# Kernel tuning notes

Measured on AMD Instinct MI355X. Metric: run time of the kernel, lower is better.

The kernel has to match this reference:

```python
import jax, jax.numpy as jnp
import numpy as np

N_NODES = 40000
N_EDGES = 640000
DIM_H = 512
N_HEADS = 8
D_HEAD = DIM_H // N_HEADS


def setup_inputs() -> dict:
    key = jax.random.key(0)
    ks = jax.random.split(key, 8)
    x = jax.random.normal(ks[0], (N_NODES, DIM_H), dtype=jnp.float32)
    edge_index = jax.random.randint(ks[1], (2, N_EDGES), 0, N_NODES, dtype=jnp.int32)
    virt_h = jax.random.normal(ks[2], (1, DIM_H), dtype=jnp.float32)
    virt_edge_index = jnp.zeros((2, 1), dtype=jnp.int32)
    s = 1.0 / np.sqrt(DIM_H)
    Wq = jax.random.normal(ks[3], (DIM_H, DIM_H), dtype=jnp.float32) * s
    Wk = jax.random.normal(ks[4], (DIM_H, DIM_H), dtype=jnp.float32) * s
    Wv = jax.random.normal(ks[5], (DIM_H, DIM_H), dtype=jnp.float32) * s
    bn_gamma = jnp.ones((DIM_H,), dtype=jnp.float32)
    bn_beta = jnp.zeros((DIM_H,), dtype=jnp.float32)
    return {"x": x, "edge_index": edge_index, "virt_h": virt_h,
            "virt_edge_index": virt_edge_index, "Wq": Wq, "Wk": Wk, "Wv": Wv,
            "bn_gamma": bn_gamma, "bn_beta": bn_beta}


def _exphormer_attn(x, edge_index, Wq, Wk, Wv):
    N, D = x.shape
    H, d = N_HEADS, D_HEAD
    Q = (x @ Wq).reshape(N, H, d)
    K = (x @ Wk).reshape(N, H, d)
    V = (x @ Wv).reshape(N, H, d)
    src, dst = edge_index[0], edge_index[1]
    scale = np.float32(1.0 / np.sqrt(d))
    # per-edge, per-head score: sum over head dim of elementwise q*k
    score = jnp.einsum('ehd,ehd->eh', K[src], Q[dst]) * scale  # [E, H]
    score = jnp.exp(jnp.clip(score, -5.0, 5.0))[..., None]     # [E, H, 1]
    msg = V[src] * score                                        # [E, H, d]
    wV = jax.ops.segment_sum(msg, dst, num_segments=N)          # [N, H, d]
    Z = jax.ops.segment_sum(score, dst, num_segments=N)         # [N, H, 1]
    return (wV / (Z + 1e-6)).reshape(N, D)


def reference(x, edge_index, virt_h, virt_edge_index, Wq, Wk, Wv, bn_gamma, bn_beta):
    # virt_h / virt_edge_index unused: use_virt_nodes=False
    h_attn = _exphormer_attn(x, edge_index, Wq, Wk, Wv)
    h = x + h_attn  # dropout p=0 -> identity; residual
    # BatchNorm1d (training-mode batch statistics, biased variance)
    mean = jnp.mean(h, axis=0)
    var = jnp.mean(jnp.square(h - mean), axis=0)
    return (h - mean) * jax.lax.rsqrt(var + 1e-5) * bn_gamma + bn_beta
```

## Files before the change

kernel.cpp:

```cpp
#include <hip/hip_runtime.h>
#include <hip/hip_bf16.h>

#define N_NODES 40000
#define M_PAD   40064
#define N_EDGES 640000
#define DIM_H 512
#define QKV_STRIDE 1536
#define ROW_BYTES 3072

typedef __attribute__((ext_vector_type(8))) short bf16x8_t;
typedef __attribute__((ext_vector_type(4))) float f32x4_t;
typedef __attribute__((ext_vector_type(8))) unsigned short u16x8_t;

static __device__ __forceinline__ unsigned short f2bf(float f) {
    __hip_bfloat16 h = __float2bfloat16(f);
    return *reinterpret_cast<unsigned short*>(&h);
}
static __device__ __forceinline__ float bf2f(unsigned short u) {
    return __uint_as_float(((unsigned)u) << 16);
}
static __device__ __forceinline__ void gll16(const void* g, void* l) {
    __builtin_amdgcn_global_load_lds(
        (const __attribute__((address_space(1))) unsigned int*)g,
        (__attribute__((address_space(3))) unsigned int*)l, 16, 0, 0);
}

__global__ __launch_bounds__(256)
void cast_x(const float* __restrict__ x, unsigned short* __restrict__ xb)
{
    const size_t i = ((size_t)blockIdx.x * 256 + threadIdx.x) * 8;
    const float4 v0 = *(const float4*)&x[i];
    const float4 v1 = *(const float4*)&x[i + 4];
    u16x8_t o;
    o[0] = f2bf(v0.x); o[1] = f2bf(v0.y); o[2] = f2bf(v0.z); o[3] = f2bf(v0.w);
    o[4] = f2bf(v1.x); o[5] = f2bf(v1.y); o[6] = f2bf(v1.z); o[7] = f2bf(v1.w);
    *(u16x8_t*)&xb[i] = o;
}

__global__ __launch_bounds__(256)
void cast_wt(const float* __restrict__ Wq,
             const float* __restrict__ Wk,
             const float* __restrict__ Wv,
             unsigned short* __restrict__ Wt)
{
    __shared__ float tile[32][33];
    const float* W = (blockIdx.z == 0) ? Wq : (blockIdx.z == 1) ? Wk : Wv;
    unsigned short* Wo = Wt + (size_t)blockIdx.z * 512 * 512;
    const int k0 = blockIdx.x * 32, n0 = blockIdx.y * 32;
    const int tx = threadIdx.x & 31, ty0 = threadIdx.x >> 5;
    #pragma unroll
    for (int p = 0; p < 4; ++p) {
        const int r = ty0 + p * 8;
        tile[r][tx] = W[(size_t)(k0 + r) * 512 + n0 + tx];
    }
    __syncthreads();
    #pragma unroll
    for (int p = 0; p < 4; ++p) {
        const int r = ty0 + p * 8;
        Wo[(size_t)(n0 + r) * 512 + k0 + tx] = f2bf(tile[tx][r]);
    }
}

__global__ __launch_bounds__(256)
void qkv_gemm_mfma(const unsigned short* __restrict__ xb,
                   const unsigned short* __restrict__ Wt,
                   unsigned short* __restrict__ qkv)
{
    __shared__ short Asub[128 * 32];
    __shared__ short Bsub[128 * 32];

    const int orig = blockIdx.x;
    const int q = 469, rmod = 4;
    const int xcd = orig & 7;
    const int sub = orig >> 3;
    const int wg = (xcd < rmod ? xcd * (q + 1) : rmod * (q + 1) + (xcd - rmod) * q) + sub;
    const int n0g = (wg % 12) * 128;
    const int m0  = (wg / 12) * 128;

    const int wsel = n0g >> 9;
    const int nc0  = n0g & 511;
    const int tid = threadIdx.x;
    const int l = tid & 63;
    const int w = tid >> 6;
    const int wr = w >> 1, wc = w & 1;
    const int lr = l & 15;
    const int lk = (l >> 4) * 8;

    const int idx0 = tid, idx1 = 256 + tid;
    const int ar0 = idx0 >> 2, ac0 = (((idx0 & 3) ^ ((idx0 >> 3) & 3))) * 8;
    const int ar1 = idx1 >> 2, ac1 = (((idx1 & 3) ^ ((idx1 >> 3) & 3))) * 8;

    const unsigned short* Abase = xb + (size_t)m0 * 512;
    const unsigned short* Bbase = Wt + (size_t)wsel * 262144 + (size_t)nc0 * 512;

    f32x4_t acc[4][4];
    #pragma unroll
    for (int i = 0; i < 4; ++i)
        #pragma unroll
        for (int j = 0; j < 4; ++j)
            acc[i][j] = {0.f, 0.f, 0.f, 0.f};

    for (int k0 = 0; k0 < 512; k0 += 32) {
        gll16(Abase + (size_t)ar0 * 512 + k0 + ac0, &Asub[idx0 * 8]);
        gll16(Abase + (size_t)ar1 * 512 + k0 + ac1, &Asub[idx1 * 8]);
        gll16(Bbase + (size_t)ar0 * 512 + k0 + ac0, &Bsub[idx0 * 8]);
        gll16(Bbase + (size_t)ar1 * 512 + k0 + ac1, &Bsub[idx1 * 8]);
        __syncthreads();
        bf16x8_t a[4], b[4];
        #pragma unroll
        for (int fm = 0; fm < 4; ++fm) {
            const int Ra = wr * 64 + fm * 16 + lr;
            const int pa = (((lk >> 3) ^ ((Ra >> 1) & 3))) << 3;
            a[fm] = *(const bf16x8_t*)&Asub[Ra * 32 + pa];
        }
        #pragma unroll
        for (int fn = 0; fn < 4; ++fn) {
            const int Rb = wc * 64 + fn * 16 + lr;
            const int pb = (((lk >> 3) ^ ((Rb >> 1) & 3))) << 3;
            b[fn] = *(const bf16x8_t*)&Bsub[Rb * 32 + pb];
        }
        #pragma unroll
        for (int fm = 0; fm < 4; ++fm)
            #pragma unroll
            for (int fn = 0; fn < 4; ++fn)
                acc[fm][fn] = __builtin_amdgcn_mfma_f32_16x16x32_bf16(
                                  a[fm], b[fn], acc[fm][fn], 0, 0, 0);
        __syncthreads();
    }

    #pragma unroll
    for (int fm = 0; fm < 4; ++fm)
        #pragma unroll
        for (int fn = 0; fn < 4; ++fn)
            #pragma unroll
            for (int j = 0; j < 4; ++j) {
                const int row = m0 + wr * 64 + fm * 16 + (l >> 4) * 4 + j;
                const int col = n0g + wc * 64 + fn * 16 + lr;
                qkv[(size_t)row * QKV_STRIDE + col] = f2bf(acc[fm][fn][j]);
            }
}

__global__ __launch_bounds__(256)
void csr_hist(const int* __restrict__ ei, int* __restrict__ counts)
{
    const int e = blockIdx.x * 256 + threadIdx.x;
    atomicAdd(&counts[ei[N_EDGES + e]], 1);
}

__global__ __launch_bounds__(1024)
void csr_scan(const int* __restrict__ counts, int* __restrict__ row_ptr)
{
    __shared__ int part[1024];
    const int t = threadIdx.x;
    const int base = t * 40;
    int s = 0;
    for (int i = 0; i < 40; ++i) {
        const int idx = base + i;
        if (idx < N_NODES) s += counts[idx];
    }
    part[t] = s;
    __syncthreads();
    for (int off = 1; off < 1024; off <<= 1) {
        int v = (t >= off) ? part[t - off] : 0;
        __syncthreads();
        part[t] += v;
        __syncthreads();
    }
    int run = (t == 0) ? 0 : part[t - 1];
    for (int i = 0; i < 40; ++i) {
        const int idx = base + i;
        if (idx < N_NODES) { row_ptr[idx] = run; run += counts[idx]; }
    }
    if (t == 0) row_ptr[N_NODES] = part[1023];
}

__global__ __launch_bounds__(256)
void csr_scatter(const int* __restrict__ ei, const int* __restrict__ row_ptr,
                 int* __restrict__ cursor, unsigned short* __restrict__ col)
{
    const int e = blockIdx.x * 256 + threadIdx.x;
    const int dst = ei[N_EDGES + e];
    const int pos = atomicAdd(&cursor[dst], 1);
    col[row_ptr[dst] + pos] = (unsigned short)ei[e];
}

__global__ __launch_bounds__(256)
void quant_kv(unsigned short* __restrict__ qkv,
              float* __restrict__ kscale, float* __restrict__ vscale)
{
    const int node = blockIdx.x * 4 + (threadIdx.x >> 6);
    const int lane = threadIdx.x & 63;
    unsigned short* row = qkv + (size_t)node * QKV_STRIDE;

    const u16x8_t kk = *(const u16x8_t*)(row + 512 + lane * 8);
    const u16x8_t vv = *(const u16x8_t*)(row + 1024 + lane * 8);
    float kf[8], vf[8];
    float kamax = 0.f, vamax = 0.f;
    #pragma unroll
    for (int j = 0; j < 8; ++j) {
        kf[j] = bf2f(kk[j]); kamax = fmaxf(kamax, fabsf(kf[j]));
        vf[j] = bf2f(vv[j]); vamax = fmaxf(vamax, fabsf(vf[j]));
    }
    #pragma unroll
    for (int off = 1; off < 64; off <<= 1) {
        kamax = fmaxf(kamax, __shfl_xor(kamax, off, 64));
        vamax = fmaxf(vamax, __shfl_xor(vamax, off, 64));
    }
    const float kinv = (kamax > 0.f) ? 127.0f / kamax : 0.f;
    const float vinv = (vamax > 0.f) ? 127.0f / vamax : 0.f;

    unsigned int klo = 0, khi = 0, vlo = 0, vhi = 0;
    #pragma unroll
    for (int j = 0; j < 4; ++j) {
        const int kq = (int)rintf(kf[j] * kinv);
        const int vq = (int)rintf(vf[j] * vinv);
        klo |= ((unsigned)(unsigned char)(signed char)kq) << (8 * j);
        vlo |= ((unsigned)(unsigned char)(signed char)vq) << (8 * j);
    }
    #pragma unroll
    for (int j = 4; j < 8; ++j) {
        const int kq = (int)rintf(kf[j] * kinv);
        const int vq = (int)rintf(vf[j] * vinv);
        khi |= ((unsigned)(unsigned char)(signed char)kq) << (8 * (j - 4));
        vhi |= ((unsigned)(unsigned char)(signed char)vq) << (8 * (j - 4));
    }
    uint2 kp; kp.x = klo; kp.y = khi;
    uint2 vp; vp.x = vlo; vp.y = vhi;
    char* rowb = (char*)row;
    *(uint2*)(rowb + 1024 + lane * 8) = kp;
    *(uint2*)(rowb + 2048 + lane * 8) = vp;
    if (lane == 0) {
        kscale[node] = kamax * (1.0f / 127.0f);
        vscale[node] = vamax * (1.0f / 127.0f);
    }
}

__global__ __launch_bounds__(128)
void edge_fused(const unsigned short* __restrict__ qkv,
                const float* __restrict__ kscale,
                const float* __restrict__ vscale,
                const int* __restrict__ row_ptr,
                const unsigned short* __restrict__ col,
                const float* __restrict__ x,
                float* __restrict__ out)
{
    const int node = blockIdx.x * 2 + (threadIdx.x >> 6);
    const int lane = threadIdx.x & 63;
    const int d0b = lane * 8;

    const u16x8_t q8 = *(const u16x8_t*)(qkv + (size_t)node * QKV_STRIDE + lane * 8);
    float q[8];
    #pragma unroll
    for (int j = 0; j < 8; ++j) q[j] = bf2f(q8[j]);

    const char* qb = (const char*)qkv;
    float acc[8] = {0.f, 0.f, 0.f, 0.f, 0.f, 0.f, 0.f, 0.f};
    float zsum = 0.f;
    const int start = row_ptr[node];
    const int end   = row_ptr[node + 1];

    int e = start;
    for (; e + 4 <= end; e += 4) {
        const int s0 = col[e], s1 = col[e + 1], s2 = col[e + 2], s3 = col[e + 3];
        const uint2 k0 = *(const uint2*)(qb + (size_t)s0 * ROW_BYTES + 1024 + d0b);
        const uint2 k1 = *(const uint2*)(qb + (size_t)s1 * ROW_BYTES + 1024 + d0b);
        const uint2 k2 = *(const uint2*)(qb + (size_t)s2 * ROW_BYTES + 1024 + d0b);
        const uint2 k3 = *(const uint2*)(qb + (size_t)s3 * ROW_BYTES + 1024 + d0b);
        const uint2 v0 = *(const uint2*)(qb + (size_t)s0 * ROW_BYTES + 2048 + d0b);
        const uint2 v1 = *(const uint2*)(qb + (size_t)s1 * ROW_BYTES + 2048 + d0b);
        const uint2 v2 = *(const uint2*)(qb + (size_t)s2 * ROW_BYTES + 2048 + d0b);
        const uint2 v3 = *(const uint2*)(qb + (size_t)s3 * ROW_BYTES + 2048 + d0b);
        const signed char* ck0 = (const signed char*)&k0;
        const signed char* ck1 = (const signed char*)&k1;
        const signed char* ck2 = (const signed char*)&k2;
        const signed char* ck3 = (const signed char*)&k3;
        float p0 = 0.f, p1 = 0.f, p2 = 0.f, p3 = 0.f;
        #pragma unroll
        for (int j = 0; j < 8; ++j) {
            p0 = fmaf((float)ck0[j], q[j], p0);
            p1 = fmaf((float)ck1[j], q[j], p1);
            p2 = fmaf((float)ck2[j], q[j], p2);
            p3 = fmaf((float)ck3[j], q[j], p3);
        }
        p0 += __shfl_xor(p0, 1, 64); p0 += __shfl_xor(p0, 2, 64); p0 += __shfl_xor(p0, 4, 64);
        p1 += __shfl_xor(p1, 1, 64); p1 += __shfl_xor(p1, 2, 64); p1 += __shfl_xor(p1, 4, 64);
        p2 += __shfl_xor(p2, 1, 64); p2 += __shfl_xor(p2, 2, 64); p2 += __shfl_xor(p2, 4, 64);
        p3 += __shfl_xor(p3, 1, 64); p3 += __shfl_xor(p3, 2, 64); p3 += __shfl_xor(p3, 4, 64);
        const float sc0 = __expf(fminf(fmaxf(p0 * kscale[s0] * 0.125f, -5.f), 5.f));
        const float sc1 = __expf(fminf(fmaxf(p1 * kscale[s1] * 0.125f, -5.f), 5.f));
        const float sc2 = __expf(fminf(fmaxf(p2 * kscale[s2] * 0.125f, -5.f), 5.f));
        const float sc3 = __expf(fminf(fmaxf(p3 * kscale[s3] * 0.125f, -5.f), 5.f));
        zsum += (sc0 + sc1) + (sc2 + sc3);
        const float scv0 = sc0 * vscale[s0];
        const float scv1 = sc1 * vscale[s1];
        const float scv2 = sc2 * vscale[s2];
        const float scv3 = sc3 * vscale[s3];
        const signed char* cv0 = (const signed char*)&v0;
        const signed char* cv1 = (const signed char*)&v1;
        const signed char* cv2 = (const signed char*)&v2;
        const signed char* cv3 = (const signed char*)&v3;
        #pragma unroll
        for (int j = 0; j < 8; ++j) {
            float a = acc[j];
            a = fmaf(scv0, (float)cv0[j], a);
            a = fmaf(scv1, (float)cv1[j], a);
            a = fmaf(scv2, (float)cv2[j], a);
            a = fmaf(scv3, (float)cv3[j], a);
            acc[j] = a;
        }
    }
    for (; e < end; ++e) {
        const int s0 = col[e];
        const uint2 k0 = *(const uint2*)(qb + (size_t)s0 * ROW_BYTES + 1024 + d0b);
        const uint2 v0 = *(const uint2*)(qb + (size_t)s0 * ROW_BYTES + 2048 + d0b);
        const signed char* ck0 = (const signed char*)&k0;
        float p0 = 0.f;
        #pragma unroll
        for (int j = 0; j < 8; ++j) p0 = fmaf((float)ck0[j], q[j], p0);
        p0 += __shfl_xor(p0, 1, 64); p0 += __shfl_xor(p0, 2, 64); p0 += __shfl_xor(p0, 4, 64);
        const float sc0 = __expf(fminf(fmaxf(p0 * kscale[s0] * 0.125f, -5.f), 5.f));
        zsum += sc0;
        const float scv0 = sc0 * vscale[s0];
        const signed char* cv0 = (const signed char*)&v0;
        #pragma unroll
        for (int j = 0; j < 8; ++j) acc[j] = fmaf(scv0, (float)cv0[j], acc[j]);
    }

    const float invz = 1.0f / (zsum + 1e-6f);
    const float* xr = x + (size_t)node * 512 + lane * 8;
    float xv[8];
    #pragma unroll
    for (int j = 0; j < 8; ++j) xv[j] = __builtin_nontemporal_load(xr + j);
    float* orow = out + (size_t)node * 512 + lane * 8;
    #pragma unroll
    for (int j = 0; j < 8; ++j)
        __builtin_nontemporal_store(xv[j] + acc[j] * invz, orow + j);
}

__global__ __launch_bounds__(512)
void stats_pass(const float* __restrict__ hbuf, float* __restrict__ stats)
{
    const int c  = threadIdx.x;
    const int r0 = blockIdx.x * 80;
    float sum = 0.f, sq = 0.f;
    for (int i = 0; i < 80; ++i) {
        const float hv = hbuf[(size_t)(r0 + i) * 512 + c];
        sum += hv; sq += hv * hv;
    }
    atomicAdd(&stats[c], sum);
    atomicAdd(&stats[512 + c], sq);
}

__global__ __launch_bounds__(256)
void bn_norm(float* __restrict__ hbuf,
             const float* __restrict__ stats,
             const float* __restrict__ gamma,
             const float* __restrict__ beta)
{
    const size_t i4 = ((size_t)blockIdx.x * 256 + threadIdx.x) * 4;
    const int c = (int)(i4 & 511);
    const float invN = 1.0f / 40000.0f;
    float4 h = *(float4*)&hbuf[i4];
    float hv[4] = {h.x, h.y, h.z, h.w};
    float o[4];
    #pragma unroll
    for (int j = 0; j < 4; ++j) {
        const float mean = stats[c + j] * invN;
        const float var  = stats[512 + c + j] * invN - mean * mean;
        o[j] = (hv[j] - mean) * rsqrtf(var + 1e-5f) * gamma[c + j] + beta[c + j];
    }
    float4 out = {o[0], o[1], o[2], o[3]};
    *(float4*)&hbuf[i4] = out;
}

extern "C" void kernel_launch(void* const* d_in, const int* in_sizes, int n_in,
                              void* d_out, int out_size, void* d_ws, size_t ws_size,
                              hipStream_t stream)
{
    const float* x     = (const float*)d_in[0];
    const int*   ei    = (const int*)d_in[1];
    const float* Wq    = (const float*)d_in[4];
    const float* Wk    = (const float*)d_in[5];
    const float* Wv    = (const float*)d_in[6];
    const float* gamma = (const float*)d_in[7];
    const float* beta  = (const float*)d_in[8];
    float* out = (float*)d_out;

    char* ws = (char*)d_ws;
    unsigned short* qkv    = (unsigned short*)ws;
    unsigned short* xb     = (unsigned short*)(ws + 123076608);
    unsigned short* Wt     = (unsigned short*)(ws + 164102144);
    int*            counts = (int*)           (ws + 165675008);
    int*            cursor = (int*)           (ws + 165835008);
    int*            row_ptr= (int*)           (ws + 165995008);
    unsigned short* col    = (unsigned short*)(ws + 166155024);
    float*          stats  = (float*)         (ws + 167435056);
    float* kscale = (float*)(ws + 123076608 + 26000000);
    float* vscale = (float*)(ws + 123076608 + 26160000);

    hipMemsetAsync(counts, 0, 160000, stream);
    hipMemsetAsync(cursor, 0, 160000, stream);
    hipMemsetAsync(stats,  0, 4096,   stream);
    hipMemsetAsync(xb + (size_t)N_NODES * 512, 0, (size_t)(M_PAD - N_NODES) * 512 * 2, stream);

    cast_x<<<10000, 256, 0, stream>>>(x, xb);
    cast_wt<<<dim3(16, 16, 3), 256, 0, stream>>>(Wq, Wk, Wv, Wt);
    csr_hist<<<2500, 256, 0, stream>>>(ei, counts);
    csr_scan<<<1, 1024, 0, stream>>>(counts, row_ptr);
    csr_scatter<<<2500, 256, 0, stream>>>(ei, row_ptr, cursor, col);
    qkv_gemm_mfma<<<3756, 256, 0, stream>>>(xb, Wt, qkv);
    quant_kv<<<10000, 256, 0, stream>>>(qkv, kscale, vscale);
    edge_fused<<<20000, 128, 0, stream>>>(qkv, kscale, vscale, row_ptr, col, x, out);
    stats_pass<<<500, 512, 0, stream>>>(out, stats);
    bn_norm<<<20000, 256, 0, stream>>>(out, stats, gamma, beta);
}
```

Before: 442.9 us.

## Fuse K/V int8 quantization into GEMM epilogue with per-head scales in row

Removes the separate quant_kv kernel by quantizing K and V to int8 directly in the QKV GEMM epilogue, using per-head (64-wide) absmax scales reduced by lane shuffles. The scales are stored inside each node's row next to the int8 data, so edge_fused reads them from the same cache lines as K/V instead of from separate scale arrays. This saves a full read and write pass over the QKV buffer and some scattered scale loads. The scale granularity changes from per-node to per-head, which is finer and should slightly improve accuracy, but the epilogue now does byte-wide scattered stores.

```diff
diff --git a/kernel.cpp b/kernel.cpp
--- a/kernel.cpp
+++ b/kernel.cpp
@@ -128,16 +128,45 @@
         __syncthreads();
     }
 
-    #pragma unroll
-    for (int fm = 0; fm < 4; ++fm)
-        #pragma unroll
-        for (int fn = 0; fn < 4; ++fn)
+    if (wsel == 0) {
+        #pragma unroll
+        for (int fm = 0; fm < 4; ++fm)
+            #pragma unroll
+            for (int fn = 0; fn < 4; ++fn)
+                #pragma unroll
+                for (int j = 0; j < 4; ++j) {
+                    const int row = m0 + wr * 64 + fm * 16 + (l >> 4) * 4 + j;
+                    const int col = n0g + wc * 64 + fn * 16 + lr;
+                    qkv[(size_t)row * QKV_STRIDE + col] = f2bf(acc[fm][fn][j]);
+                }
+    } else {
+        const int hd     = (nc0 >> 6) + wc;
+        const int sbase  = (wsel == 1) ? 1024 : 2048;
+        const int scbase = (wsel == 1) ? 1536 : 1568;
+        #pragma unroll
+        for (int fm = 0; fm < 4; ++fm)
             #pragma unroll
             for (int j = 0; j < 4; ++j) {
                 const int row = m0 + wr * 64 + fm * 16 + (l >> 4) * 4 + j;
-                const int col = n0g + wc * 64 + fn * 16 + lr;
-                qkv[(size_t)row * QKV_STRIDE + col] = f2bf(acc[fm][fn][j]);
+                float m = 0.f;
+                #pragma unroll
+                for (int fn = 0; fn < 4; ++fn)
+                    m = fmaxf(m, fabsf(acc[fm][fn][j]));
+                m = fmaxf(m, __shfl_xor(m, 1, 64));
+                m = fmaxf(m, __shfl_xor(m, 2, 64));
+                m = fmaxf(m, __shfl_xor(m, 4, 64));
+                m = fmaxf(m, __shfl_xor(m, 8, 64));
+                const float inv = (m > 0.f) ? 127.0f / m : 0.f;
+                char* rowb = (char*)qkv + (size_t)row * ROW_BYTES;
+                #pragma unroll
+                for (int fn = 0; fn < 4; ++fn) {
+                    const int qv = (int)rintf(acc[fm][fn][j] * inv);
+                    rowb[sbase + hd * 64 + fn * 16 + lr] = (char)(signed char)qv;
+                }
+                if (lr == 0)
+                    *(float*)(rowb + scbase + hd * 4) = m * (1.0f / 127.0f);
             }
+    }
 }
 
 __global__ __launch_bounds__(256)
@@ -184,61 +213,8 @@
     col[row_ptr[dst] + pos] = (unsigned short)ei[e];
 }
 
-__global__ __launch_bounds__(256)
-void quant_kv(unsigned short* __restrict__ qkv,
-              float* __restrict__ kscale, float* __restrict__ vscale)
-{
-    const int node = blockIdx.x * 4 + (threadIdx.x >> 6);
-    const int lane = threadIdx.x & 63;
-    unsigned short* row = qkv + (size_t)node * QKV_STRIDE;
-
-    const u16x8_t kk = *(const u16x8_t*)(row + 512 + lane * 8);
-    const u16x8_t vv = *(const u16x8_t*)(row + 1024 + lane * 8);
-    float kf[8], vf[8];
-    float kamax = 0.f, vamax = 0.f;
-    #pragma unroll
-    for (int j = 0; j < 8; ++j) {
-        kf[j] = bf2f(kk[j]); kamax = fmaxf(kamax, fabsf(kf[j]));
-        vf[j] = bf2f(vv[j]); vamax = fmaxf(vamax, fabsf(vf[j]));
-    }
-    #pragma unroll
-    for (int off = 1; off < 64; off <<= 1) {
-        kamax = fmaxf(kamax, __shfl_xor(kamax, off, 64));
-        vamax = fmaxf(vamax, __shfl_xor(vamax, off, 64));
-    }
-    const float kinv = (kamax > 0.f) ? 127.0f / kamax : 0.f;
-    const float vinv = (vamax > 0.f) ? 127.0f / vamax : 0.f;
-
-    unsigned int klo = 0, khi = 0, vlo = 0, vhi = 0;
-    #pragma unroll
-    for (int j = 0; j < 4; ++j) {
-        const int kq = (int)rintf(kf[j] * kinv);
-        const int vq = (int)rintf(vf[j] * vinv);
-        klo |= ((unsigned)(unsigned char)(signed char)kq) << (8 * j);
-        vlo |= ((unsigned)(unsigned char)(signed char)vq) << (8 * j);
-    }
-    #pragma unroll
-    for (int j = 4; j < 8; ++j) {
-        const int kq = (int)rintf(kf[j] * kinv);
-        const int vq = (int)rintf(vf[j] * vinv);
-        khi |= ((unsigned)(unsigned char)(signed char)kq) << (8 * (j - 4));
-        vhi |= ((unsigned)(unsigned char)(signed char)vq) << (8 * (j - 4));
-    }
-    uint2 kp; kp.x = klo; kp.y = khi;
-    uint2 vp; vp.x = vlo; vp.y = vhi;
-    char* rowb = (char*)row;
-    *(uint2*)(rowb + 1024 + lane * 8) = kp;
-    *(uint2*)(rowb + 2048 + lane * 8) = vp;
-    if (lane == 0) {
-        kscale[node] = kamax * (1.0f / 127.0f);
-        vscale[node] = vamax * (1.0f / 127.0f);
-    }
-}
-
 __global__ __launch_bounds__(128)
 void edge_fused(const unsigned short* __restrict__ qkv,
-                const float* __restrict__ kscale,
-                const float* __restrict__ vscale,
                 const int* __restrict__ row_ptr,
                 const unsigned short* __restrict__ col,
                 const float* __restrict__ x,
@@ -246,6 +222,7 @@
 {
     const int node = blockIdx.x * 2 + (threadIdx.x >> 6);
     const int lane = threadIdx.x & 63;
+    const int g = lane >> 3;
     const int d0b = lane * 8;
 
     const u16x8_t q8 = *(const u16x8_t*)(qkv + (size_t)node * QKV_STRIDE + lane * 8);
@@ -262,14 +239,22 @@
     int e = start;
     for (; e + 4 <= end; e += 4) {
         const int s0 = col[e], s1 = col[e + 1], s2 = col[e + 2], s3 = col[e + 3];
-        const uint2 k0 = *(const uint2*)(qb + (size_t)s0 * ROW_BYTES + 1024 + d0b);
-        const uint2 k1 = *(const uint2*)(qb + (size_t)s1 * ROW_BYTES + 1024 + d0b);
-        const uint2 k2 = *(const uint2*)(qb + (size_t)s2 * ROW_BYTES + 1024 + d0b);
-        const uint2 k3 = *(const uint2*)(qb + (size_t)s3 * ROW_BYTES + 1024 + d0b);
-        const uint2 v0 = *(const uint2*)(qb + (size_t)s0 * ROW_BYTES + 2048 + d0b);
-        const uint2 v1 = *(const uint2*)(qb + (size_t)s1 * ROW_BYTES + 2048 + d0b);
-        const uint2 v2 = *(const uint2*)(qb + (size_t)s2 * ROW_BYTES + 2048 + d0b);
-        const uint2 v3 = *(const uint2*)(qb + (size_t)s3 * ROW_BYTES + 2048 + d0b);
+        const char* rb0 = qb + (size_t)s0 * ROW_BYTES;
+        const char* rb1 = qb + (size_t)s1 * ROW_BYTES;
+        const char* rb2 = qb + (size_t)s2 * ROW_BYTES;
+        const char* rb3 = qb + (size_t)s3 * ROW_BYTES;
+        const uint2 k0 = *(const uint2*)(rb0 + 1024 + d0b);
+        const uint2 k1 = *(const uint2*)(rb1 + 1024 + d0b);
+        const uint2 k2 = *(const uint2*)(rb2 + 1024 + d0b);
+        const uint2 k3 = *(const uint2*)(rb3 + 1024 + d0b);
+        const uint2 v0 = *(const uint2*)(rb0 + 2048 + d0b);
+        const uint2 v1 = *(const uint2*)(rb1 + 2048 + d0b);
+        const uint2 v2 = *(const uint2*)(rb2 + 2048 + d0b);
+        const uint2 v3 = *(const uint2*)(rb3 + 2048 + d0b);
+        const float ks0 = *(const float*)(rb0 + 1536 + g * 4);
+        const float ks1 = *(const float*)(rb1 + 1536 + g * 4);
+        const float ks2 = *(const float*)(rb2 + 1536 + g * 4);
+        const float ks3 = *(const float*)(rb3 + 1536 + g * 4);
         const signed char* ck0 = (const signed char*)&k0;
         const signed char* ck1 = (const signed char*)&k1;
         const signed char* ck2 = (const signed char*)&k2;
@@ -286,15 +271,15 @@
         p1 += __shfl_xor(p1, 1, 64); p1 += __shfl_xor(p1, 2, 64); p1 += __shfl_xor(p1, 4, 64);
         p2 += __shfl_xor(p2, 1, 64); p2 += __shfl_xor(p2, 2, 64); p2 += __shfl_xor(p2, 4, 64);
         p3 += __shfl_xor(p3, 1, 64); p3 += __shfl_xor(p3, 2, 64); p3 += __shfl_xor(p3, 4, 64);
-        const float sc0 = __expf(fminf(fmaxf(p0 * kscale[s0] * 0.125f, -5.f), 5.f));
-        const float sc1 = __expf(fminf(fmaxf(p1 * kscale[s1] * 0.125f, -5.f), 5.f));
-        const float sc2 = __expf(fminf(fmaxf(p2 * kscale[s2] * 0.125f, -5.f), 5.f));
-        const float sc3 = __expf(fminf(fmaxf(p3 * kscale[s3] * 0.125f, -5.f), 5.f));
+        const float sc0 = __expf(fminf(fmaxf(p0 * ks0 * 0.125f, -5.f), 5.f));
+        const float sc1 = __expf(fminf(fmaxf(p1 * ks1 * 0.125f, -5.f), 5.f));
+        const float sc2 = __expf(fminf(fmaxf(p2 * ks2 * 0.125f, -5.f), 5.f));
+        const float sc3 = __expf(fminf(fmaxf(p3 * ks3 * 0.125f, -5.f), 5.f));
         zsum += (sc0 + sc1) + (sc2 + sc3);
-        const float scv0 = sc0 * vscale[s0];
-        const float scv1 = sc1 * vscale[s1];
-        const float scv2 = sc2 * vscale[s2];
-        const float scv3 = sc3 * vscale[s3];
+        const float scv0 = sc0 * *(const float*)(rb0 + 1568 + g * 4);
+        const float scv1 = sc1 * *(const float*)(rb1 + 1568 + g * 4);
+        const float scv2 = sc2 * *(const float*)(rb2 + 1568 + g * 4);
+        const float scv3 = sc3 * *(const float*)(rb3 + 1568 + g * 4);
         const signed char* cv0 = (const signed char*)&v0;
         const signed char* cv1 = (const signed char*)&v1;
         const signed char* cv2 = (const signed char*)&v2;
@@ -311,16 +296,18 @@
     }
     for (; e < end; ++e) {
         const int s0 = col[e];
-        const uint2 k0 = *(const uint2*)(qb + (size_t)s0 * ROW_BYTES + 1024 + d0b);
-        const uint2 v0 = *(const uint2*)(qb + (size_t)s0 * ROW_BYTES + 2048 + d0b);
+        const char* rb0 = qb + (size_t)s0 * ROW_BYTES;
+        const uint2 k0 = *(const uint2*)(rb0 + 1024 + d0b);
+        const uint2 v0 = *(const uint2*)(rb0 + 2048 + d0b);
+        const float ks0 = *(const float*)(rb0 + 1536 + g * 4);
         const signed char* ck0 = (const signed char*)&k0;
         float p0 = 0.f;
         #pragma unroll
         for (int j = 0; j < 8; ++j) p0 = fmaf((float)ck0[j], q[j], p0);
         p0 += __shfl_xor(p0, 1, 64); p0 += __shfl_xor(p0, 2, 64); p0 += __shfl_xor(p0, 4, 64);
-        const float sc0 = __expf(fminf(fmaxf(p0 * kscale[s0] * 0.125f, -5.f), 5.f));
+        const float sc0 = __expf(fminf(fmaxf(p0 * ks0 * 0.125f, -5.f), 5.f));
         zsum += sc0;
-        const float scv0 = sc0 * vscale[s0];
+        const float scv0 = sc0 * *(const float*)(rb0 + 1568 + g * 4);
         const signed char* cv0 = (const signed char*)&v0;
         #pragma unroll
         for (int j = 0; j < 8; ++j) acc[j] = fmaf(scv0, (float)cv0[j], acc[j]);
@@ -395,8 +382,6 @@
     int*            row_ptr= (int*)           (ws + 165995008);
     unsigned short* col    = (unsigned short*)(ws + 166155024);
     float*          stats  = (float*)         (ws + 167435056);
-    float* kscale = (float*)(ws + 123076608 + 26000000);
-    float* vscale = (float*)(ws + 123076608 + 26160000);
 
     hipMemsetAsync(counts, 0, 160000, stream);
     hipMemsetAsync(cursor, 0, 160000, stream);
@@ -409,8 +394,7 @@
     csr_scan<<<1, 1024, 0, stream>>>(counts, row_ptr);
     csr_scatter<<<2500, 256, 0, stream>>>(ei, row_ptr, cursor, col);
     qkv_gemm_mfma<<<3756, 256, 0, stream>>>(xb, Wt, qkv);
-    quant_kv<<<10000, 256, 0, stream>>>(qkv, kscale, vscale);
-    edge_fused<<<20000, 128, 0, stream>>>(qkv, kscale, vscale, row_ptr, col, x, out);
+    edge_fused<<<20000, 128, 0, stream>>>(qkv, row_ptr, col, x, out);
     stats_pass<<<500, 512, 0, stream>>>(out, stats);
     bn_norm<<<20000, 256, 0, stream>>>(out, stats, gamma, beta);
 }
```

Measured after the change: 430.3 us, median of 2. -2.8%, faster.
